# Optimization experiments

Measured on AMD Instinct MI355X. Metric: run time of the kernel, lower is better.

## Reference

```python
import jax, jax.numpy as jnp
import numpy as np

B, N, S, H = 128, 512, 8, 64
HORIZON = 12


def setup_inputs() -> dict:
    key = jax.random.key(0)
    ks = jax.random.split(key, 24)
    sc = 0.05
    inp = {
        "crowd_obsv": jax.random.normal(ks[0], (B, N, S, 2), jnp.float32),
        "pad_mask": jax.random.bernoulli(ks[1], 0.9, (B, N, N)),
        "neg_hist_mask": jnp.ones((B, N, S, 1), jnp.float32),
        # LSTM params (PyTorch layout, gate order i,f,g,o)
        "Wih": jax.random.normal(ks[2], (4 * H, 2), jnp.float32) * sc,
        "Whh": jax.random.normal(ks[3], (4 * H, H), jnp.float32) * sc,
        "bih": jax.random.normal(ks[4], (4 * H,), jnp.float32) * sc,
        "bhh": jax.random.normal(ks[5], (4 * H,), jnp.float32) * sc,
        # human_encoder: ReLU, Linear, ReLU, Linear, ReLU
        "W_enc1": jax.random.normal(ks[6], (H, H), jnp.float32) * sc,
        "b_enc1": jax.random.normal(ks[7], (H,), jnp.float32) * sc,
        "W_enc2": jax.random.normal(ks[8], (H, H), jnp.float32) * sc,
        "b_enc2": jax.random.normal(ks[9], (H,), jnp.float32) * sc,
        # human_head: Linear, ReLU
        "W_head": jax.random.normal(ks[10], (H, H), jnp.float32) * sc,
        "b_head": jax.random.normal(ks[11], (H,), jnp.float32) * sc,
        "Wq": jax.random.normal(ks[12], (H, H), jnp.float32) * sc,
        "bq": jax.random.normal(ks[13], (H,), jnp.float32) * sc,
        "Wk": jax.random.normal(ks[14], (H, H), jnp.float32) * sc,
        "bk": jax.random.normal(ks[15], (H,), jnp.float32) * sc,
        "Wv": jax.random.normal(ks[16], (H, H), jnp.float32) * sc,
        "bv": jax.random.normal(ks[17], (H,), jnp.float32) * sc,
        # human_forecaster: Linear(2H -> horizon*2)
        "Wf": jax.random.normal(ks[18], (HORIZON * 2, 2 * H), jnp.float32) * sc,
        "bf": jax.random.normal(ks[19], (HORIZON * 2,), jnp.float32) * sc,
    }
    return inp


def _forward(crowd_obsv, pad_mask, neg_hist_mask, Wih, Whh, bih, bhh,
             W_enc1, b_enc1, W_enc2, b_enc2, W_head, b_head,
             Wq, bq, Wk, bk, Wv, bv, Wf, bf):
    b, n, s, _ = crowd_obsv.shape
    h_dim = Whh.shape[1]
    horizon = Wf.shape[0] // 2

    x = (crowd_obsv * neg_hist_mask).reshape(-1, s, 2)  # [M, S, 2]
    m = x.shape[0]

    # --- variable-length masking: find last zero index (x-channel) ---
    zero_mask = (x == 0)                                  # [M, S, 2]
    ar = jnp.arange(s)
    lzi = jnp.max(zero_mask * ar[None, :, None], axis=1)  # [M, 2]
    lzi = jnp.where(zero_mask.any(axis=1), lzi, -1)
    lzi = lzi[:, 0]                                       # [M]
    rows = ar[None, :]
    kill = (rows < lzi[:, None]) & (lzi[:, None] >= 0)    # [M, S]
    x = jnp.where(kill[:, :, None], jnp.zeros((), x.dtype), x)
    length = jnp.maximum((s - 1) - lzi, 1)                # clamp(7 - lzi, min=1)

    # --- packed LSTM via masked scan: state frozen once t >= length ---
    bias = bih + bhh

    def step(carry, inp):
        h, c = carry
        xt, t = inp
        gates = xt @ Wih.T + h @ Whh.T + bias           # [M, 4H]
        i, f, g, o = jnp.split(gates, 4, axis=-1)
        c_new = jax.nn.sigmoid(f) * c + jax.nn.sigmoid(i) * jnp.tanh(g)
        h_new = jax.nn.sigmoid(o) * jnp.tanh(c_new)
        upd = (t < length)[:, None]
        return (jnp.where(upd, h_new, h), jnp.where(upd, c_new, c)), None

    init = (jnp.zeros((m, h_dim), x.dtype), jnp.zeros((m, h_dim), x.dtype))
    (hn, _), _ = jax.lax.scan(step, init, (x.transpose(1, 0, 2), jnp.arange(s)))

    he = hn.reshape(b, n, h_dim)

    # human_encoder + human_head
    h1 = jax.nn.relu(he)
    h1 = jax.nn.relu(h1 @ W_enc1.T + b_enc1)
    h1 = jax.nn.relu(h1 @ W_enc2.T + b_enc2)
    hidden = jax.nn.relu(h1 @ W_head.T + b_head)

    q = hidden @ Wq.T + bq
    k = hidden @ Wk.T + bk
    v = hidden @ Wv.T + bv

    logits = jnp.einsum('bnh,bmh->bnm', q, k)
    logits = jnp.where(pad_mask, logits, jnp.asarray(-999999999999.0, logits.dtype))
    attn = jnp.einsum('bnm,bmh->bnh', jax.nn.softmax(logits, axis=2), v)

    feat = jnp.concatenate([v, attn], axis=-1)            # [B, N, 2H]
    forecast = (feat @ Wf.T + bf).reshape(-1, n, horizon, 2)
    return forecast, feat


def reference(crowd_obsv, pad_mask, neg_hist_mask, Wih, Whh, bih, bhh,
              W_enc1, b_enc1, W_enc2, b_enc2, W_head, b_head,
              Wq, bq, Wk, bk, Wv, bv, Wf, bf):
    return _forward(crowd_obsv, pad_mask, neg_hist_mask, Wih, Whh, bih, bhh,
                    W_enc1, b_enc1, W_enc2, b_enc2, W_head, b_head,
                    Wq, bq, Wk, bk, Wv, bv, Wf, bf)
```

## Files before the change

kernel.cpp:

```cpp
#include <hip/hip_runtime.h>
#include <hip/hip_bf16.h>
#include <stdint.h>

#define B_ 128
#define N_ 512
#define S_ 8
#define H_ 64
#define M_ (B_*N_)
#define L2E 1.442695041f

typedef __attribute__((ext_vector_type(8))) short bf16x8;
typedef __attribute__((ext_vector_type(4))) float f32x4;

__device__ __forceinline__ float exp2f_(float x) { return __builtin_amdgcn_exp2f(x); }
__device__ __forceinline__ float rcpf_(float x)  { return __builtin_amdgcn_rcpf(x); }
__device__ __forceinline__ float sig2(float x)  { return rcpf_(1.f + exp2f_(-x)); }
__device__ __forceinline__ float tanh2(float x) { return 1.f - 2.f*rcpf_(exp2f_(x) + 1.f); }
__device__ __forceinline__ unsigned short f2bf(float x) {
  unsigned int u = __float_as_uint(x);
  u += 0x7fffu + ((u >> 16) & 1u);
  return (unsigned short)(u >> 16);
}

__global__ __launch_bounds__(512, 4) void lstm_kernel(
    const float* __restrict__ obs, const float* __restrict__ nhm,
    const float* __restrict__ Wih, const float* __restrict__ Whh,
    const float* __restrict__ bih, const float* __restrict__ bhh,
    unsigned short* __restrict__ he,
    const int4* __restrict__ pm4, uint32_t* __restrict__ bm)
{
  __shared__ short    Wfrag[32*512];
  __shared__ short    Wxc[1024];
  __shared__ short    h_s[128*72];

  const int tid  = threadIdx.x;
  const int lane = tid & 63;
  const int wv   = tid >> 6;
  const int w16  = wv * 16;
  const int quad = lane >> 4;
  const int col  = lane & 15;
  const int row0 = blockIdx.x * 128;

  const int     wb  = (blockIdx.x*8 + wv) * 256;
  const int4*   pw  = pm4 + (size_t)wb * 8;
  const int     shp = (lane & 7) * 4;

  #pragma unroll
  for (int i = 0; i < 4; ++i) {
    int p = i*512 + tid;
    int f = p >> 6, l = p & 63;
    int t16 = f >> 1, s = f & 1;
    int lq = l >> 4, lc = l & 15;
    const float sc = (t16 >= 8 && t16 < 12) ? (2.f*L2E) : L2E;
    const float* src = Whh + (size_t)(t16*16 + lc)*64 + s*32 + lq*8;
    short* dst = Wfrag + f*512 + l*8;
    #pragma unroll
    for (int j = 0; j < 8; ++j) dst[j] = (short)f2bf(src[j] * sc);
  }
  if (tid < 256) {
    int t16 = tid >> 4, cc = tid & 15;
    int n = t16*16 + cc;
    const float sc = (t16 >= 8 && t16 < 12) ? (2.f*L2E) : L2E;
    short* d = Wxc + t16*64 + cc*4;
    d[0] = (short)f2bf(Wih[2*n + 0] * sc);
    d[1] = (short)f2bf(Wih[2*n + 1] * sc);
    d[2] = (short)f2bf((bih[n] + bhh[n]) * sc);
    d[3] = 0;
  }

  #pragma unroll
  for (int i = 0; i < 9; ++i) ((uint32_t*)h_s)[i*512 + tid] = 0u;

  uint32_t xq0, xq1, xq2, xq3, xq4, xq5, xq6, xq7;
  int len;
  {
    const int grow = row0 + w16 + col;
    float xv0[8], xv1[8];
    int lzi = -1;
    #pragma unroll
    for (int t = 0; t < 8; ++t) {
      float m = nhm[(size_t)grow*8 + t];
      float a = obs[((size_t)grow*8 + t)*2 + 0] * m;
      float b = obs[((size_t)grow*8 + t)*2 + 1] * m;
      xv0[t] = a; xv1[t] = b;
      if (a == 0.f) lzi = t;
    }
    uint32_t xr[8];
    #pragma unroll
    for (int t = 0; t < 8; ++t) {
      bool kill = (t < lzi);
      float a = kill ? 0.f : xv0[t];
      float b = kill ? 0.f : xv1[t];
      xr[t] = (uint32_t)f2bf(a) | ((uint32_t)f2bf(b) << 16);
    }
    xq0 = xr[0]; xq1 = xr[1]; xq2 = xr[2]; xq3 = xr[3];
    xq4 = xr[4]; xq5 = xr[5]; xq6 = xr[6]; xq7 = xr[7];
    len = 7 - lzi; if (len < 1) len = 1;
  }
  int lenr[4];
  #pragma unroll
  for (int r = 0; r < 4; ++r) lenr[r] = __shfl(len, quad*4 + r);

  __syncthreads();

  float c_[16];
  #pragma unroll
  for (int i = 0; i < 16; ++i) c_[i] = 0.f;

  const f32x4 zero4 = {0.f, 0.f, 0.f, 0.f};
  const bool q0 = (quad == 0);

  #pragma unroll 1
  for (int t = 0; t < 8; ++t) {
    const int4* ps = pw + t*256 + lane;
    int4 pv0 = ps[0];
    int4 pv1 = ps[64];
    int4 pv2 = ps[128];
    int4 pv3 = ps[192];
    __builtin_amdgcn_sched_barrier(0);

    uint32_t xw = xq0;
    xq0 = xq1; xq1 = xq2; xq2 = xq3; xq3 = xq4;
    xq4 = xq5; xq5 = xq6; xq6 = xq7;

    union { bf16x8 v; uint32_t u[4]; } ax;
    ax.u[0] = q0 ? xw : 0u;
    ax.u[1] = q0 ? 0x00003f80u : 0u;
    ax.u[2] = 0u; ax.u[3] = 0u;

    bf16x8 a0 = *(const bf16x8*)(h_s + (w16 + col)*72 + quad*8);
    bf16x8 a1 = *(const bf16x8*)(h_s + (w16 + col)*72 + 32 + quad*8);

    #pragma unroll
    for (int cc = 0; cc < 4; ++cc) {
      f32x4 acc[4];
      #pragma unroll
      for (int g = 0; g < 4; ++g) {
        const int t16 = g*4 + cc;
        union { bf16x8 v; uint32_t u[4]; } wx;
        uint2 d = *(const uint2*)(Wxc + t16*64 + col*4);
        wx.u[0] = q0 ? d.x : 0u;
        wx.u[1] = q0 ? d.y : 0u;
        wx.u[2] = 0u; wx.u[3] = 0u;
        bf16x8 b0 = *(const bf16x8*)(Wfrag + (t16*2+0)*512 + lane*8);
        bf16x8 b1 = *(const bf16x8*)(Wfrag + (t16*2+1)*512 + lane*8);
        acc[g] = __builtin_amdgcn_mfma_f32_16x16x32_bf16(ax.v, wx.v, zero4, 0, 0, 0);
        acc[g] = __builtin_amdgcn_mfma_f32_16x16x32_bf16(a0, b0, acc[g], 0, 0, 0);
        acc[g] = __builtin_amdgcn_mfma_f32_16x16x32_bf16(a1, b1, acc[g], 0, 0, 0);
      }
      #pragma unroll
      for (int r = 0; r < 4; ++r) {
        if (t < lenr[r]) {
          float gi = acc[0][r];
          float gf = acc[1][r];
          float gg = acc[2][r];
          float go = acc[3][r];
          float cn = sig2(gf)*c_[cc*4+r] + sig2(gi)*tanh2(gg);
          c_[cc*4+r] = cn;
          h_s[(w16 + quad*4 + r)*72 + cc*16 + col] =
              (short)f2bf(sig2(go)*tanh2(cn*(2.f*L2E)));
        }
      }
      __builtin_amdgcn_sched_barrier(0);
    }

    {
      int4 vv[4] = {pv0, pv1, pv2, pv3};
      #pragma unroll
      for (int jj = 0; jj < 4; ++jj) {
        int4 v = vv[jj];
        uint32_t nib = (v.x != 0 ? 1u : 0u)
                     | (v.y != 0 ? 2u : 0u)
                     | (v.z != 0 ? 4u : 0u)
                     | (v.w != 0 ? 8u : 0u);
        uint32_t x = nib << shp;
        x |= __shfl_xor(x, 1);
        x |= __shfl_xor(x, 2);
        x |= __shfl_xor(x, 4);
        if ((lane & 7) == 0)
          bm[wb + t*32 + jj*8 + (lane >> 3)] = x;
      }
      __builtin_amdgcn_sched_barrier(0);
    }
  }

  #pragma unroll
  for (int s = 0; s < 2; ++s) {
    int chunk = s*64 + lane;
    int rl = chunk >> 3, c8 = chunk & 7;
    bf16x8 v = *(const bf16x8*)(h_s + (w16 + rl)*72 + c8*8);
    #pragma unroll
    for (int j = 0; j < 8; ++j) {
      short sv = v[j];
      v[j] = (sv & (short)0x8000) ? (short)0 : sv;
    }
    *(bf16x8*)(he + (size_t)(row0 + w16 + rl)*64 + c8*8) = v;
  }
}

__global__ __launch_bounds__(256) void mlp_kernel(
    const unsigned short* __restrict__ he,
    const float* __restrict__ W1, const float* __restrict__ b1,
    const float* __restrict__ W2, const float* __restrict__ b2,
    const float* __restrict__ Wh, const float* __restrict__ bh,
    const float* __restrict__ Wq, const float* __restrict__ bq,
    const float* __restrict__ Wk, const float* __restrict__ bk,
    const float* __restrict__ Wv, const float* __restrict__ bv,
    unsigned short* __restrict__ qb, unsigned short* __restrict__ kb,
    unsigned short* __restrict__ vt, float* __restrict__ feat)
{
  __shared__ short Wm[3][8*512];
  __shared__ float bias_s[6*64];
  __shared__ short Atile[4][16*76];

  const int tid  = threadIdx.x;
  const int lane = tid & 63;
  const int wv   = tid >> 6;
  const int quad = lane >> 4;
  const int col  = lane & 15;
  const int rowb = blockIdx.x*64 + wv*16;

  const float* m1[3] = {W1, W2, Wh};
  const float* m2[3] = {Wq, Wk, Wv};
  auto stage3 = [&](const float* const* mats, float sc0) {
    #pragma unroll
    for (int i = 0; i < 6; ++i) {
      int p = i*256 + tid;
      int m = p >> 9, rem = p & 511;
      int f = rem >> 6, l = rem & 63;
      int nt = f >> 1, s = f & 1;
      int lq = l >> 4, lc = l & 15;
      float sc = (m == 0) ? sc0 : 1.f;
      const float* src = mats[m] + (size_t)(nt*16 + lc)*64 + s*32 + lq*8;
      short* dst = &Wm[m][f*512 + l*8];
      #pragma unroll
      for (int j = 0; j < 8; ++j) dst[j] = (short)f2bf(src[j] * sc);
    }
  };
  stage3(m1, 1.f);
  {
    const float* bs[6] = {b1, b2, bh, bq, bk, bv};
    for (int i = tid; i < 384; i += 256) {
      float sc = ((i >> 6) == 3) ? L2E : 1.f;
      bias_s[i] = bs[i>>6][i & 63] * sc;
    }
  }
  __syncthreads();

  bf16x8 a0 = *(const bf16x8*)(he + (size_t)(rowb + col)*64 + quad*8);
  bf16x8 a1 = *(const bf16x8*)(he + (size_t)(rowb + col)*64 + quad*8 + 32);

  f32x4 acc[4];
  auto runL = [&](int m, int bidx) {
    #pragma unroll
    for (int nt = 0; nt < 4; ++nt) {
      float bb = bias_s[bidx*64 + nt*16 + col];
      acc[nt][0] = bb; acc[nt][1] = bb; acc[nt][2] = bb; acc[nt][3] = bb;
    }
    #pragma unroll
    for (int nt = 0; nt < 4; ++nt) {
      bf16x8 bf0 = *(const bf16x8*)(&Wm[m][(nt*2+0)*512 + lane*8]);
      bf16x8 bf1 = *(const bf16x8*)(&Wm[m][(nt*2+1)*512 + lane*8]);
      acc[nt] = __builtin_amdgcn_mfma_f32_16x16x32_bf16(a0, bf0, acc[nt], 0,0,0);
      acc[nt] = __builtin_amdgcn_mfma_f32_16x16x32_bf16(a1, bf1, acc[nt], 0,0,0);
    }
  };
  auto tileWrite = [&](bool relu) {
    #pragma unroll
    for (int nt = 0; nt < 4; ++nt)
      #pragma unroll
      for (int r = 0; r < 4; ++r) {
        float v = relu ? fmaxf(acc[nt][r], 0.f) : acc[nt][r];
        Atile[wv][(quad*4+r)*76 + ((nt*16+col) ^ (r*16))] = (short)f2bf(v);
      }
  };
  auto tileReadA = [&]() {
    int sw = (col & 3) * 16;
    a0 = *(const bf16x8*)(&Atile[wv][col*76 + ((quad*8     ) ^ sw)]);
    a1 = *(const bf16x8*)(&Atile[wv][col*76 + ((quad*8 + 32) ^ sw)]);
  };
  auto storeBF = [&](unsigned short* dst) {
    #pragma unroll
    for (int s = 0; s < 2; ++s) {
      int chunk = s*64 + lane;
      int r = chunk >> 3, c8 = chunk & 7;
      bf16x8 v = *(const bf16x8*)(&Atile[wv][r*76 + ((c8*8) ^ ((r&3)*16))]);
      *(bf16x8*)(dst + (size_t)(rowb + r)*64 + c8*8) = v;
    }
  };

  runL(0, 0); tileWrite(true); tileReadA();
  runL(1, 1); tileWrite(true); tileReadA();
  runL(2, 2); tileWrite(true); tileReadA();
  __syncthreads();
  stage3(m2, L2E);
  __syncthreads();

  runL(0, 3); tileWrite(false); storeBF(qb);
  runL(1, 4); tileWrite(false); storeBF(kb);
  runL(2, 5);
  {
    const int bi   = rowb >> 9;
    const int key0 = (rowb & 511) + quad*4;
    #pragma unroll
    for (int nt = 0; nt < 4; ++nt) {
      #pragma unroll
      for (int r = 0; r < 4; ++r)
        feat[(size_t)(rowb + quad*4 + r)*128 + nt*16 + col] = acc[nt][r];
      uint32_t lo = (uint32_t)f2bf(acc[nt][0]) | ((uint32_t)f2bf(acc[nt][1]) << 16);
      uint32_t hi = (uint32_t)f2bf(acc[nt][2]) | ((uint32_t)f2bf(acc[nt][3]) << 16);
      uint2 pk; pk.x = lo; pk.y = hi;
      *(uint2*)(vt + ((size_t)bi*64 + nt*16 + col)*512 + key0) = pk;
    }
  }
}

__global__ __launch_bounds__(256) void attn_kernel(
    const unsigned short* __restrict__ qg, const unsigned short* __restrict__ kg,
    const unsigned short* __restrict__ vt,
    const uint32_t* __restrict__ bm, float* __restrict__ feat,
    const float* __restrict__ Wf, const float* __restrict__ bfv,
    float* __restrict__ out)
{
  __shared__ short    Ks[128*72];
  __shared__ short    Vt[64*136];
  __shared__ short    Pl[4][16*32];
  __shared__ uint32_t Ms[4][256];
  __shared__ short    Wfr[8*512];
  __shared__ float    bl[32];

  const int tid  = threadIdx.x;
  const int lane = tid & 63;
  const int wv   = tid >> 6;
  const int w16  = wv * 16;
  const int quad = lane >> 4;
  const int col  = lane & 15;

  const int b     = blockIdx.x >> 3;
  const int q0    = (blockIdx.x & 7) * 64;
  const int qbase = b*512 + q0 + wv*16;

  bf16x8 qa[2];
  qa[0] = *(const bf16x8*)(qg + (size_t)(qbase + col)*64 + quad*8);
  qa[1] = *(const bf16x8*)(qg + (size_t)(qbase + col)*64 + quad*8 + 32);

  #pragma unroll
  for (int w = 0; w < 4; ++w)
    Ms[wv][w*64 + lane] = bm[(size_t)qbase*16 + w*64 + lane];

  #pragma unroll
  for (int i = 0; i < 2; ++i) {
    int p = i*256 + tid;
    int f = p >> 6, l = p & 63;
    int kc = f >> 1, nt = f & 1;
    int lq = l >> 4, lc = l & 15;
    int n = nt*16 + lc;
    bf16x8 v;
    #pragma unroll
    for (int j = 0; j < 8; ++j) v[j] = 0;
    if (n < 24) {
      const float* src = Wf + (size_t)n*128 + kc*32 + lq*8;
      #pragma unroll
      for (int j = 0; j < 8; ++j) v[j] = (short)f2bf(src[j]);
    }
    *(bf16x8*)(Wfr + f*512 + l*8) = v;
  }
  if (tid < 32) bl[tid] = (tid < 24) ? bfv[tid] : 0.f;

  f32x4 o_acc[4];
  #pragma unroll
  for (int nt = 0; nt < 4; ++nt)
    #pragma unroll
    for (int r = 0; r < 4; ++r) o_acc[nt][r] = 0.f;
  float l_part[4] = {0.f, 0.f, 0.f, 0.f};

  const unsigned short* vtb = vt + (size_t)b*64*512;

  for (int c = 0; c < 4; ++c) {
    __syncthreads();
    {
      const int kb_ = b*512 + c*128;
      #pragma unroll
      for (int i = 0; i < 4; ++i) {
        int p = i*256 + tid;
        int key = p >> 3, c8 = p & 7;
        bf16x8 kv = *(const bf16x8*)(kg + (size_t)(kb_ + key)*64 + c8*8);
        *(bf16x8*)(Ks + key*72 + c8*8) = kv;
      }
      #pragma unroll
      for (int i = 0; i < 4; ++i) {
        int p = i*256 + tid;
        int dim = p >> 4, k8 = p & 15;
        bf16x8 vv = *(const bf16x8*)(vtb + (size_t)dim*512 + c*128 + k8*8);
        *(bf16x8*)(Vt + dim*136 + k8*8) = vv;
      }
    }
    __syncthreads();

    for (int kc = 0; kc < 4; ++kc) {
      #pragma unroll
      for (int t = 0; t < 2; ++t) {
        const int kt = kc*2 + t;
        f32x4 s_acc;
        #pragma unroll
        for (int r = 0; r < 4; ++r) s_acc[r] = 0.f;
        const short* kp = Ks + (kt*16 + col)*72 + quad*8;
        bf16x8 kb0 = *(const bf16x8*)(kp);
        bf16x8 kb1 = *(const bf16x8*)(kp + 32);
        s_acc = __builtin_amdgcn_mfma_f32_16x16x32_bf16(qa[0], kb0, s_acc, 0,0,0);
        s_acc = __builtin_amdgcn_mfma_f32_16x16x32_bf16(qa[1], kb1, s_acc, 0,0,0);
        const int kcol = ((t*16 + col) ^ (quad*8));
        #pragma unroll
        for (int r = 0; r < 4; ++r) {
          uint32_t mw = Ms[wv][(quad*4+r)*16 + c*4 + (kt>>1)];
          float p = ((mw >> ((kt&1)*16 + col)) & 1u)
                      ? exp2f_(fminf(s_acc[r], 43.f)) : 0.f;
          l_part[r] += p;
          Pl[wv][(quad*4+r)*32 + kcol] = (short)f2bf(p);
        }
      }
      bf16x8 pa = *(const bf16x8*)(&Pl[wv][col*32 + ((quad*8) ^ (((col)>>2)*8))]);
      #pragma unroll
      for (int nt = 0; nt < 4; ++nt) {
        bf16x8 vb = *(const bf16x8*)(&Vt[(nt*16+col)*136 + kc*32 + quad*8]);
        o_acc[nt] = __builtin_amdgcn_mfma_f32_16x16x32_bf16(pa, vb, o_acc[nt], 0,0,0);
      }
    }
  }

  float inv[4];
  #pragma unroll
  for (int r = 0; r < 4; ++r) {
    float v = l_part[r];
    v += __shfl_xor(v, 1);
    v += __shfl_xor(v, 2);
    v += __shfl_xor(v, 4);
    v += __shfl_xor(v, 8);
    inv[r] = rcpf_(fmaxf(v, 1e-20f));
  }

  #pragma unroll
  for (int nt = 0; nt < 4; ++nt)
    #pragma unroll
    for (int r = 0; r < 4; ++r)
      feat[(size_t)(qbase + quad*4 + r)*128 + 64 + nt*16 + col] = o_acc[nt][r]*inv[r];

  __syncthreads();

  #pragma unroll
  for (int nt = 0; nt < 4; ++nt)
    #pragma unroll
    for (int r = 0; r < 4; ++r)
      Ks[(w16 + quad*4 + r)*72 + nt*16 + col] = (short)f2bf(o_acc[nt][r]*inv[r]);

  bf16x8 af[4];
  const float* fr = feat + (size_t)(qbase + col)*128;
  #pragma unroll
  for (int kc = 0; kc < 2; ++kc) {
    float4 f0 = *(const float4*)(fr + kc*32 + quad*8);
    float4 f1 = *(const float4*)(fr + kc*32 + quad*8 + 4);
    af[kc][0]=(short)f2bf(f0.x); af[kc][1]=(short)f2bf(f0.y);
    af[kc][2]=(short)f2bf(f0.z); af[kc][3]=(short)f2bf(f0.w);
    af[kc][4]=(short)f2bf(f1.x); af[kc][5]=(short)f2bf(f1.y);
    af[kc][6]=(short)f2bf(f1.z); af[kc][7]=(short)f2bf(f1.w);
  }
  #pragma unroll
  for (int kc = 2; kc < 4; ++kc)
    af[kc] = *(const bf16x8*)(Ks + (w16 + col)*72 + (kc-2)*32 + quad*8);

  f32x4 facc[2];
  #pragma unroll
  for (int nt = 0; nt < 2; ++nt) {
    float bb = bl[nt*16 + col];
    facc[nt][0] = bb; facc[nt][1] = bb; facc[nt][2] = bb; facc[nt][3] = bb;
  }
  #pragma unroll
  for (int kc = 0; kc < 4; ++kc) {
    #pragma unroll
    for (int nt = 0; nt < 2; ++nt) {
      bf16x8 bfr = *(const bf16x8*)(Wfr + (kc*2+nt)*512 + lane*8);
      facc[nt] = __builtin_amdgcn_mfma_f32_16x16x32_bf16(af[kc], bfr, facc[nt], 0,0,0);
    }
  }

  #pragma unroll
  for (int nt = 0; nt < 2; ++nt) {
    int n = nt*16 + col;
    if (n < 24) {
      #pragma unroll
      for (int r = 0; r < 4; ++r)
        out[(size_t)(qbase + quad*4 + r)*24 + n] = facc[nt][r];
    }
  }
}

extern "C" void kernel_launch(void* const* d_in, const int* in_sizes, int n_in,
                              void* d_out, int out_size, void* d_ws, size_t ws_size,
                              hipStream_t stream)
{
  const float* obs = (const float*)d_in[0];
  const int*   pm  = (const int*)  d_in[1];
  const float* nhm = (const float*)d_in[2];
  const float* Wih = (const float*)d_in[3];
  const float* Whh = (const float*)d_in[4];
  const float* bih = (const float*)d_in[5];
  const float* bhh = (const float*)d_in[6];
  const float* W1  = (const float*)d_in[7];
  const float* b1  = (const float*)d_in[8];
  const float* W2  = (const float*)d_in[9];
  const float* b2  = (const float*)d_in[10];
  const float* Wh  = (const float*)d_in[11];
  const float* bh  = (const float*)d_in[12];
  const float* Wq  = (const float*)d_in[13];
  const float* bq  = (const float*)d_in[14];
  const float* Wk  = (const float*)d_in[15];
  const float* bk  = (const float*)d_in[16];
  const float* Wv  = (const float*)d_in[17];
  const float* bv  = (const float*)d_in[18];
  const float* Wf  = (const float*)d_in[19];
  const float* bf  = (const float*)d_in[20];

  float* out  = (float*)d_out;
  float* feat = out + (size_t)M_*24;

  char* ws = (char*)d_ws;
  unsigned short* he  = (unsigned short*)(ws);
  unsigned short* qbf = (unsigned short*)(ws + (size_t) 8*1024*1024);
  unsigned short* kbf = (unsigned short*)(ws + (size_t)16*1024*1024);
  unsigned short* vtb = (unsigned short*)(ws + (size_t)24*1024*1024);
  uint32_t*       bmw = (uint32_t*)      (ws + (size_t)32*1024*1024);

  lstm_kernel<<<M_/128, 512, 0, stream>>>(obs, nhm, Wih, Whh, bih, bhh, he,
                                          (const int4*)pm, bmw);
  mlp_kernel<<<M_/64, 256, 0, stream>>>(he, W1,b1, W2,b2, Wh,bh, Wq,bq, Wk,bk, Wv,bv,
                                        qbf, kbf, vtb, feat);
  attn_kernel<<<M_/64, 256, 0, stream>>>(qbf, kbf, vtb, bmw, feat, Wf, bf, out);
}
```

Measured before the change: 309.0 us.

## Pre-pack bf16 weight fragments once in LSTM kernel, read from global downstream

The first seven LSTM blocks convert the MLP, QKV and forecaster weights into bf16 MFMA fragment layout and write them to a workspace buffer. The MLP and attention kernels then load these fragments straight from global memory instead of having every block convert fp32 weights into shared memory. This drops per-block staging work, shared-memory use and two barriers from the MLP kernel, which may help occupancy. In exchange, fragments are re-read from global/L2 on every layer, and the Wq scaling path converts twice.

```diff
diff --git a/kernel.cpp b/kernel.cpp
--- a/kernel.cpp
+++ b/kernel.cpp
@@ -27,7 +27,11 @@
     const float* __restrict__ Wih, const float* __restrict__ Whh,
     const float* __restrict__ bih, const float* __restrict__ bhh,
     unsigned short* __restrict__ he,
-    const int4* __restrict__ pm4, uint32_t* __restrict__ bm)
+    const int4* __restrict__ pm4, uint32_t* __restrict__ bm,
+    const float* __restrict__ W1, const float* __restrict__ W2,
+    const float* __restrict__ Wh, const float* __restrict__ Wq,
+    const float* __restrict__ Wk, const float* __restrict__ Wv,
+    const float* __restrict__ Wf, unsigned short* __restrict__ wg)
 {
   __shared__ short    Wfrag[32*512];
   __shared__ short    Wxc[1024];
@@ -70,6 +74,37 @@
 
   #pragma unroll
   for (int i = 0; i < 9; ++i) ((uint32_t*)h_s)[i*512 + tid] = 0u;
+
+  if (blockIdx.x < 7) {
+    const int m = blockIdx.x;
+    const int p = tid;
+    const int f = p >> 6, l = p & 63;
+    const int lq = l >> 4, lc = l & 15;
+    bf16x8 v;
+    #pragma unroll
+    for (int j = 0; j < 8; ++j) v[j] = 0;
+    if (m < 6) {
+      const float* mats[6] = {W1, W2, Wh, Wq, Wk, Wv};
+      const float sc = (m == 3) ? L2E : 1.f;
+      const int nt = f >> 1, s = f & 1;
+      const float* src = mats[m] + (size_t)(nt*16 + lc)*64 + s*32 + lq*8;
+      #pragma unroll
+      for (int j = 0; j < 8; ++j) v[j] = (short)f2bf(src[j]);
+      if (m == 3) {
+        #pragma unroll
+        for (int j = 0; j < 8; ++j) v[j] = (short)f2bf(src[j] * sc);
+      }
+    } else {
+      const int kc = f >> 1, nt = f & 1;
+      const int n = nt*16 + lc;
+      if (n < 24) {
+        const float* src = Wf + (size_t)n*128 + kc*32 + lq*8;
+        #pragma unroll
+        for (int j = 0; j < 8; ++j) v[j] = (short)f2bf(src[j]);
+      }
+    }
+    *(bf16x8*)(wg + (size_t)m*4096 + f*512 + l*8) = v;
+  }
 
   uint32_t xq0, xq1, xq2, xq3, xq4, xq5, xq6, xq7;
   int len;
@@ -199,18 +234,13 @@
 }
 
 __global__ __launch_bounds__(256) void mlp_kernel(
-    const unsigned short* __restrict__ he,
-    const float* __restrict__ W1, const float* __restrict__ b1,
-    const float* __restrict__ W2, const float* __restrict__ b2,
-    const float* __restrict__ Wh, const float* __restrict__ bh,
-    const float* __restrict__ Wq, const float* __restrict__ bq,
-    const float* __restrict__ Wk, const float* __restrict__ bk,
-    const float* __restrict__ Wv, const float* __restrict__ bv,
+    const unsigned short* __restrict__ he, const unsigned short* __restrict__ wg,
+    const float* __restrict__ b1, const float* __restrict__ b2,
+    const float* __restrict__ bh, const float* __restrict__ bq,
+    const float* __restrict__ bk, const float* __restrict__ bv,
     unsigned short* __restrict__ qb, unsigned short* __restrict__ kb,
     unsigned short* __restrict__ vt, float* __restrict__ feat)
 {
-  __shared__ short Wm[3][8*512];
-  __shared__ float bias_s[6*64];
   __shared__ short Atile[4][16*76];
 
   const int tid  = threadIdx.x;
@@ -220,49 +250,21 @@
   const int col  = lane & 15;
   const int rowb = blockIdx.x*64 + wv*16;
 
-  const float* m1[3] = {W1, W2, Wh};
-  const float* m2[3] = {Wq, Wk, Wv};
-  auto stage3 = [&](const float* const* mats, float sc0) {
-    #pragma unroll
-    for (int i = 0; i < 6; ++i) {
-      int p = i*256 + tid;
-      int m = p >> 9, rem = p & 511;
-      int f = rem >> 6, l = rem & 63;
-      int nt = f >> 1, s = f & 1;
-      int lq = l >> 4, lc = l & 15;
-      float sc = (m == 0) ? sc0 : 1.f;
-      const float* src = mats[m] + (size_t)(nt*16 + lc)*64 + s*32 + lq*8;
-      short* dst = &Wm[m][f*512 + l*8];
-      #pragma unroll
-      for (int j = 0; j < 8; ++j) dst[j] = (short)f2bf(src[j] * sc);
-    }
-  };
-  stage3(m1, 1.f);
-  {
-    const float* bs[6] = {b1, b2, bh, bq, bk, bv};
-    for (int i = tid; i < 384; i += 256) {
-      float sc = ((i >> 6) == 3) ? L2E : 1.f;
-      bias_s[i] = bs[i>>6][i & 63] * sc;
-    }
-  }
-  __syncthreads();
-
   bf16x8 a0 = *(const bf16x8*)(he + (size_t)(rowb + col)*64 + quad*8);
   bf16x8 a1 = *(const bf16x8*)(he + (size_t)(rowb + col)*64 + quad*8 + 32);
 
   f32x4 acc[4];
-  auto runL = [&](int m, int bidx) {
+  auto runL = [&](int m, const float* __restrict__ bs, float bsc) {
+    bf16x8 bf[8];
+    #pragma unroll
+    for (int f = 0; f < 8; ++f)
+      bf[f] = *(const bf16x8*)(wg + (size_t)m*4096 + f*512 + lane*8);
     #pragma unroll
     for (int nt = 0; nt < 4; ++nt) {
-      float bb = bias_s[bidx*64 + nt*16 + col];
+      float bb = bs[nt*16 + col] * bsc;
       acc[nt][0] = bb; acc[nt][1] = bb; acc[nt][2] = bb; acc[nt][3] = bb;
-    }
-    #pragma unroll
-    for (int nt = 0; nt < 4; ++nt) {
-      bf16x8 bf0 = *(const bf16x8*)(&Wm[m][(nt*2+0)*512 + lane*8]);
-      bf16x8 bf1 = *(const bf16x8*)(&Wm[m][(nt*2+1)*512 + lane*8]);
-      acc[nt] = __builtin_amdgcn_mfma_f32_16x16x32_bf16(a0, bf0, acc[nt], 0,0,0);
-      acc[nt] = __builtin_amdgcn_mfma_f32_16x16x32_bf16(a1, bf1, acc[nt], 0,0,0);
+      acc[nt] = __builtin_amdgcn_mfma_f32_16x16x32_bf16(a0, bf[nt*2+0], acc[nt], 0,0,0);
+      acc[nt] = __builtin_amdgcn_mfma_f32_16x16x32_bf16(a1, bf[nt*2+1], acc[nt], 0,0,0);
     }
   };
   auto tileWrite = [&](bool relu) {
@@ -289,16 +291,12 @@
     }
   };
 
-  runL(0, 0); tileWrite(true); tileReadA();
-  runL(1, 1); tileWrite(true); tileReadA();
-  runL(2, 2); tileWrite(true); tileReadA();
-  __syncthreads();
-  stage3(m2, L2E);
-  __syncthreads();
-
-  runL(0, 3); tileWrite(false); storeBF(qb);
-  runL(1, 4); tileWrite(false); storeBF(kb);
-  runL(2, 5);
+  runL(0, b1, 1.f);  tileWrite(true);  tileReadA();
+  runL(1, b2, 1.f);  tileWrite(true);  tileReadA();
+  runL(2, bh, 1.f);  tileWrite(true);  tileReadA();
+  runL(3, bq, L2E);  tileWrite(false); storeBF(qb);
+  runL(4, bk, 1.f);  tileWrite(false); storeBF(kb);
+  runL(5, bv, 1.f);
   {
     const int bi   = rowb >> 9;
     const int key0 = (rowb & 511) + quad*4;
@@ -319,15 +317,13 @@
     const unsigned short* __restrict__ qg, const unsigned short* __restrict__ kg,
     const unsigned short* __restrict__ vt,
     const uint32_t* __restrict__ bm, float* __restrict__ feat,
-    const float* __restrict__ Wf, const float* __restrict__ bfv,
+    const unsigned short* __restrict__ wg, const float* __restrict__ bfv,
     float* __restrict__ out)
 {
   __shared__ short    Ks[128*72];
   __shared__ short    Vt[64*136];
   __shared__ short    Pl[4][16*32];
   __shared__ uint32_t Ms[4][256];
-  __shared__ short    Wfr[8*512];
-  __shared__ float    bl[32];
 
   const int tid  = threadIdx.x;
   const int lane = tid & 63;
@@ -347,25 +343,6 @@
   #pragma unroll
   for (int w = 0; w < 4; ++w)
     Ms[wv][w*64 + lane] = bm[(size_t)qbase*16 + w*64 + lane];
-
-  #pragma unroll
-  for (int i = 0; i < 2; ++i) {
-    int p = i*256 + tid;
-    int f = p >> 6, l = p & 63;
-    int kc = f >> 1, nt = f & 1;
-    int lq = l >> 4, lc = l & 15;
-    int n = nt*16 + lc;
-    bf16x8 v;
-    #pragma unroll
-    for (int j = 0; j < 8; ++j) v[j] = 0;
-    if (n < 24) {
-      const float* src = Wf + (size_t)n*128 + kc*32 + lq*8;
-      #pragma unroll
-      for (int j = 0; j < 8; ++j) v[j] = (short)f2bf(src[j]);
-    }
-    *(bf16x8*)(Wfr + f*512 + l*8) = v;
-  }
-  if (tid < 32) bl[tid] = (tid < 24) ? bfv[tid] : 0.f;
 
   f32x4 o_acc[4];
   #pragma unroll
@@ -471,14 +448,15 @@
   f32x4 facc[2];
   #pragma unroll
   for (int nt = 0; nt < 2; ++nt) {
-    float bb = bl[nt*16 + col];
+    int n = nt*16 + col;
+    float bb = (n < 24) ? bfv[n] : 0.f;
     facc[nt][0] = bb; facc[nt][1] = bb; facc[nt][2] = bb; facc[nt][3] = bb;
   }
   #pragma unroll
   for (int kc = 0; kc < 4; ++kc) {
     #pragma unroll
     for (int nt = 0; nt < 2; ++nt) {
-      bf16x8 bfr = *(const bf16x8*)(Wfr + (kc*2+nt)*512 + lane*8);
+      bf16x8 bfr = *(const bf16x8*)(wg + (size_t)6*4096 + (kc*2+nt)*512 + lane*8);
       facc[nt] = __builtin_amdgcn_mfma_f32_16x16x32_bf16(af[kc], bfr, facc[nt], 0,0,0);
     }
   }
@@ -529,10 +507,12 @@
   unsigned short* kbf = (unsigned short*)(ws + (size_t)16*1024*1024);
   unsigned short* vtb = (unsigned short*)(ws + (size_t)24*1024*1024);
   uint32_t*       bmw = (uint32_t*)      (ws + (size_t)32*1024*1024);
+  unsigned short* wgb = (unsigned short*)(ws + (size_t)36*1024*1024);
 
   lstm_kernel<<<M_/128, 512, 0, stream>>>(obs, nhm, Wih, Whh, bih, bhh, he,
-                                          (const int4*)pm, bmw);
-  mlp_kernel<<<M_/64, 256, 0, stream>>>(he, W1,b1, W2,b2, Wh,bh, Wq,bq, Wk,bk, Wv,bv,
+                                          (const int4*)pm, bmw,
+                                          W1, W2, Wh, Wq, Wk, Wv, Wf, wgb);
+  mlp_kernel<<<M_/64, 256, 0, stream>>>(he, wgb, b1, b2, bh, bq, bk, bv,
                                         qbf, kbf, vtb, feat);
-  attn_kernel<<<M_/64, 256, 0, stream>>>(qbf, kbf, vtb, bmw, feat, Wf, bf, out);
+  attn_kernel<<<M_/64, 256, 0, stream>>>(qbf, kbf, vtb, bmw, feat, wgb, bf, out);
 }
```

Measured after the change: 302.9 us. 2.0% less time.
